# Kernel optimization log

Hardware: AMD Instinct MI355X
Metric: run time of the kernel (lower is better)

## Reference

```python
import jax, jax.numpy as jnp
import numpy as np

N_NODES = 50000
N_EDGES = 600000
DIM_H = 128
LN_EPS = 1e-5


def setup_inputs() -> dict:
    key = jax.random.key(0)
    ks = jax.random.split(key, 8)
    s = 1.0 / np.sqrt(DIM_H)
    return {
        "nodes": jax.random.normal(ks[0], (N_NODES, DIM_H), jnp.float32),
        "W_msg": jax.random.normal(ks[1], (DIM_H, DIM_H), jnp.float32) * s,
        "b_msg": jnp.zeros((DIM_H,), jnp.float32),
        "w_ih": jax.random.normal(ks[2], (3 * DIM_H, DIM_H), jnp.float32) * s,
        "w_hh": jax.random.normal(ks[3], (3 * DIM_H, DIM_H), jnp.float32) * s,
        "b_ih": jnp.zeros((3 * DIM_H,), jnp.float32),
        "b_hh": jnp.zeros((3 * DIM_H,), jnp.float32),
        "ln_gamma": jnp.ones((DIM_H,), jnp.float32),
        "ln_beta": jnp.zeros((DIM_H,), jnp.float32),
        "edge_src": jax.random.randint(ks[4], (N_EDGES,), 0, N_NODES, jnp.int32),
        "edge_dst": jax.random.randint(ks[5], (N_EDGES,), 0, N_NODES, jnp.int32),
    }


def _layer_norm(x, gamma, beta):
    mu = jnp.mean(x, axis=-1, keepdims=True)
    var = jnp.mean(jnp.square(x - mu), axis=-1, keepdims=True)
    return gamma * (x - mu) * jax.lax.rsqrt(var + LN_EPS) + beta


def reference(nodes, W_msg, b_msg, w_ih, w_hh, b_ih, b_hh, ln_gamma, ln_beta,
              edge_src, edge_dst):
    n_nodes = nodes.shape[0]
    # send_and_recv: per-edge message from source node, sum-reduce at dest
    msg_e = nodes[edge_src] @ W_msg.T + b_msg            # [E, H] (irregular gather)
    messages = jax.ops.segment_sum(msg_e, edge_dst, num_segments=n_nodes)  # [N, H]
    # global connection: add mean node feature
    msg = messages + jnp.mean(nodes, axis=0)
    # single-step GRU (torch gate layout: r, z, n)
    gi = msg @ w_ih.T + b_ih                             # [N, 3H]
    gh = nodes @ w_hh.T + b_hh                           # [N, 3H]
    i_r, i_z, i_n = jnp.split(gi, 3, axis=-1)
    h_r, h_z, h_n = jnp.split(gh, 3, axis=-1)
    r = jax.nn.sigmoid(i_r + h_r)
    z = jax.nn.sigmoid(i_z + h_z)
    n = jnp.tanh(i_n + r * h_n)
    h_next = (1.0 - z) * n + z * nodes
    # LayerNorm then post-GRU spatial residual with messages
    out = _layer_norm(h_next, ln_gamma, ln_beta)
    out = out + messages
    return out
```

## Files before the change

kernel.cpp:

```cpp
#include <hip/hip_runtime.h>
#include <hip/hip_bf16.h>

#define N_NODES 50000
#define N_EDGES 600000
#define DIM_H   128
#define NPAD    50048
#define NB_SCAN 196

typedef __attribute__((ext_vector_type(8))) short bf16x8;
typedef __attribute__((ext_vector_type(4))) float f32x4;
typedef __attribute__((ext_vector_type(4))) short short4v;

__device__ __forceinline__ short f2bs(float f) {
    __hip_bfloat16 h = __float2bfloat16(f);
    return *reinterpret_cast<short*>(&h);
}
__device__ __forceinline__ float bs2f(short s) {
    unsigned u = ((unsigned)(unsigned short)s) << 16;
    return __builtin_bit_cast(float, u);
}
__device__ __forceinline__ float sigm(float x) { return 1.f / (1.f + __expf(-x)); }
__device__ __forceinline__ float tanh_f(float x) {
    return 2.f / (1.f + __expf(-2.f * x)) - 1.f;
}
__device__ __forceinline__ unsigned pk2(float a, float b) {
    return ((unsigned)(unsigned short)f2bs(b) << 16) | (unsigned)(unsigned short)f2bs(a);
}
__device__ __forceinline__ float unlo(unsigned u) { return bs2f((short)(u & 0xffffu)); }
__device__ __forceinline__ float unhi(unsigned u) { return bs2f((short)(u >> 16)); }

__device__ __forceinline__ void dma16(const void* g, const void* lds_uniform) {
    __builtin_amdgcn_global_load_lds(
        (const __attribute__((address_space(1))) void*)g,
        (__attribute__((address_space(3))) void*)(unsigned)(unsigned long long)lds_uniform,
        16, 0, 0);
}

__global__ __launch_bounds__(256) void prep_k(const float* __restrict__ wmsg,
                                              const float* __restrict__ wih,
                                              const float* __restrict__ whh,
                                              short* __restrict__ wmsgB,
                                              short* __restrict__ wihB,
                                              short* __restrict__ whhB,
                                              int* __restrict__ cnt,
                                              float* __restrict__ colsum,
                                              short* __restrict__ aggTail,
                                              short* __restrict__ nodesTail) {
    int i = blockIdx.x * 256 + threadIdx.x;
    if (i < 16384) wmsgB[i] = f2bs(wmsg[i]);
    if (i < 49152) { wihB[i] = f2bs(wih[i]); whhB[i] = f2bs(whh[i]); }
    if (i < N_NODES) cnt[i] = 0;
    if (i < 128) colsum[i] = 0.f;
    if (i < 1536) {
        short4v z = {0, 0, 0, 0};
        *(short4v*)(aggTail   + i * 4) = z;
        *(short4v*)(nodesTail + i * 4) = z;
    }
}

__global__ __launch_bounds__(256) void colsum_k(const float* __restrict__ nodes,
                                                float* __restrict__ colsum,
                                                short* __restrict__ nodesB) {
    __shared__ float red[8][128];
    const int tid = threadIdx.x;
    const int cg = tid & 31;
    const int rl = tid >> 5;
    float4 acc = {0.f, 0.f, 0.f, 0.f};
    for (int r = blockIdx.x * 8 + rl; r < N_NODES; r += gridDim.x * 8) {
        float4 v = *(const float4*)(nodes + (size_t)r * DIM_H + cg * 4);
        acc.x += v.x; acc.y += v.y; acc.z += v.z; acc.w += v.w;
        *(short4v*)(nodesB + (size_t)r * DIM_H + cg * 4) =
            (short4v){f2bs(v.x), f2bs(v.y), f2bs(v.z), f2bs(v.w)};
    }
    *(float4*)&red[rl][cg * 4] = acc;
    __syncthreads();
    if (tid < 128) {
        float s = 0.f;
#pragma unroll
        for (int i = 0; i < 8; ++i) s += red[i][tid];
        unsafeAtomicAdd(&colsum[tid], s);
    }
}

__global__ __launch_bounds__(256) void hist_k(const int* __restrict__ edst,
                                              int* __restrict__ cnt) {
    int e = blockIdx.x * 256 + threadIdx.x;
    if (e < N_EDGES) atomicAdd(&cnt[edst[e]], 1);
}

__global__ __launch_bounds__(256) void bsum_k(const int* __restrict__ cnt,
                                              int* __restrict__ bsum) {
    const int t = threadIdx.x;
    int i = blockIdx.x * 256 + t;
    int v = (i < N_NODES) ? cnt[i] : 0;
#pragma unroll
    for (int o = 32; o; o >>= 1) v += __shfl_xor(v, o, 64);
    __shared__ int w4[4];
    if ((t & 63) == 0) w4[t >> 6] = v;
    __syncthreads();
    if (t == 0) bsum[blockIdx.x] = w4[0] + w4[1] + w4[2] + w4[3];
}

__global__ __launch_bounds__(256) void scan2_k(const int* __restrict__ cnt,
                                               const int* __restrict__ bsum,
                                               int* __restrict__ rowptr,
                                               int* __restrict__ pos) {
    const int b = blockIdx.x, t = threadIdx.x;
    const int lane = t & 63, w = t >> 6;
    __shared__ int red[4];
    __shared__ int wsum[4];

    int ov = (t < b) ? bsum[t] : 0;
#pragma unroll
    for (int o = 32; o; o >>= 1) ov += __shfl_xor(ov, o, 64);
    if (lane == 0) red[w] = ov;
    __syncthreads();
    const int offset = red[0] + red[1] + red[2] + red[3];

    int i = b * 256 + t;
    int v = (i < N_NODES) ? cnt[i] : 0;
    int x = v;
#pragma unroll
    for (int o = 1; o < 64; o <<= 1) {
        int y = __shfl_up(x, o, 64);
        if (lane >= o) x += y;
    }
    if (lane == 63) wsum[w] = x;
    __syncthreads();
    int woff = 0;
#pragma unroll
    for (int j = 0; j < 4; ++j)
        if (j < w) woff += wsum[j];
    int excl = offset + woff + (x - v);
    if (i < N_NODES) { rowptr[i] = excl; pos[i] = excl; }
    if (i == N_NODES - 1) rowptr[N_NODES] = excl + v;
}

__global__ __launch_bounds__(256) void reorder_k(const int* __restrict__ esrc,
                                                 const int* __restrict__ edst,
                                                 int* __restrict__ pos,
                                                 int* __restrict__ ssrc) {
    int e = blockIdx.x * 256 + threadIdx.x;
    if (e < N_EDGES) {
        int p = atomicAdd(&pos[edst[e]], 1);
        ssrc[p] = esrc[e];
    }
}

__global__ __launch_bounds__(256) void aggregate_k(const short* __restrict__ nodesB,
                                                   const int* __restrict__ rowptr,
                                                   const int* __restrict__ ssrc,
                                                   short* __restrict__ aggB) {
    const int wid = threadIdx.x >> 6;
    const int lane = threadIdx.x & 63;
    const int n = blockIdx.x * 4 + wid;
    if (n >= N_NODES) return;
    const int s0 = rowptr[n], s1 = rowptr[n + 1];
    float2 acc = {0.f, 0.f};
    int e = s0;
    for (; e + 3 < s1; e += 4) {
        int sa = ssrc[e], sb = ssrc[e + 1], sc = ssrc[e + 2], sd = ssrc[e + 3];
        short2 va = ((const short2*)(nodesB + (size_t)sa * DIM_H))[lane];
        short2 vb = ((const short2*)(nodesB + (size_t)sb * DIM_H))[lane];
        short2 vc = ((const short2*)(nodesB + (size_t)sc * DIM_H))[lane];
        short2 vd = ((const short2*)(nodesB + (size_t)sd * DIM_H))[lane];
        acc.x += (bs2f(va.x) + bs2f(vb.x)) + (bs2f(vc.x) + bs2f(vd.x));
        acc.y += (bs2f(va.y) + bs2f(vb.y)) + (bs2f(vc.y) + bs2f(vd.y));
    }
    for (; e < s1; ++e) {
        int sa = ssrc[e];
        short2 va = ((const short2*)(nodesB + (size_t)sa * DIM_H))[lane];
        acc.x += bs2f(va.x);
        acc.y += bs2f(va.y);
    }
    short2 o; o.x = f2bs(acc.x); o.y = f2bs(acc.y);
    ((short2*)(aggB + (size_t)n * DIM_H))[lane] = o;
}

__global__ __launch_bounds__(256) void fused_k(const short* __restrict__ aggB,
                                               const short* __restrict__ nodesB,
                                               const short* __restrict__ wmsgB,
                                               const short* __restrict__ wihB,
                                               const short* __restrict__ whhB,
                                               const float* __restrict__ bmsg,
                                               const float* __restrict__ bih,
                                               const float* __restrict__ bhh,
                                               const int* __restrict__ deg,
                                               const float* __restrict__ colsum,
                                               const float* __restrict__ gamma,
                                               const float* __restrict__ beta,
                                               float* __restrict__ out) {
    __shared__ short Ms[64 * 128];
    __shared__ short Wb[2][64 * 128];
    __shared__ float biasL[1280];

    const int tid = threadIdx.x;
    const int lane = tid & 63, w = tid >> 6;
    const int m0 = blockIdx.x * 64;
    const int r16 = lane & 15, qh = lane >> 4;
    const int wm = w * 16;
    const float invN = 1.0f / N_NODES;

    for (int i = tid; i < 384; i += 256) {
        biasL[i]       = bih[i];
        biasL[384 + i] = bhh[i];
    }
    if (tid < 128) {
        biasL[768  + tid] = bmsg[tid];
        biasL[896  + tid] = colsum[tid] * invN;
        biasL[1024 + tid] = gamma[tid];
        biasL[1152 + tid] = beta[tid];
    }
    __syncthreads();

    bf16x8 aggF[4], nodF[4], msgF[4];
    const size_t rowA = (size_t)(m0 + wm + r16) * 128;
#pragma unroll
    for (int kt = 0; kt < 4; ++kt) {
        aggF[kt] = *(const bf16x8*)(aggB   + rowA + ((kt << 2) + qh) * 8);
        nodF[kt] = *(const bf16x8*)(nodesB + rowA + ((kt << 2) + qh) * 8);
    }
    int4 dgi = *(const int4*)(deg + m0 + wm + qh * 4);

#define STAGE_W(SRC, ROW0, BUF) do {                                         \
    _Pragma("unroll") for (int it = 0; it < 4; ++it) {                       \
        int c = w * 4 + it;                                                  \
        int s = c * 64 + lane;                                               \
        int r = s >> 4, q = s & 15;                                          \
        int g = q ^ (r & 15);                                                \
        dma16((SRC) + (((size_t)((ROW0) + r)) << 7) + (g << 3),              \
              &Wb[BUF][0] + (size_t)c * 512);                                \
    } } while (0)

    STAGE_W(wmsgB, 0, 0);

    f32x4 acc[2][4];
    unsigned rp[2][4][2], inp[2][4][2], np_[2][4][2];

#define CHUNK(BUF, AF, H, RST) do {                                          \
    _Pragma("unroll") for (int kt = 0; kt < 4; ++kt) {                       \
        const int sq = (((kt << 2) + qh) ^ r16) << 3;                        \
        bf16x8 b0 = *(const bf16x8*)&Wb[BUF][(r16     ) * 128 + sq];         \
        bf16x8 b1 = *(const bf16x8*)&Wb[BUF][(r16 + 16) * 128 + sq];         \
        bf16x8 b2 = *(const bf16x8*)&Wb[BUF][(r16 + 32) * 128 + sq];         \
        bf16x8 b3 = *(const bf16x8*)&Wb[BUF][(r16 + 48) * 128 + sq];         \
        f32x4 z4 = {0.f, 0.f, 0.f, 0.f};                                     \
        acc[H][0] = __builtin_amdgcn_mfma_f32_16x16x32_bf16(                 \
            AF[kt], b0, ((RST) && kt == 0) ? z4 : acc[H][0], 0, 0, 0);       \
        acc[H][1] = __builtin_amdgcn_mfma_f32_16x16x32_bf16(                 \
            AF[kt], b1, ((RST) && kt == 0) ? z4 : acc[H][1], 0, 0, 0);       \
        acc[H][2] = __builtin_amdgcn_mfma_f32_16x16x32_bf16(                 \
            AF[kt], b2, ((RST) && kt == 0) ? z4 : acc[H][2], 0, 0, 0);       \
        acc[H][3] = __builtin_amdgcn_mfma_f32_16x16x32_bf16(                 \
            AF[kt], b3, ((RST) && kt == 0) ? z4 : acc[H][3], 0, 0, 0);       \
    } } while (0)

    __syncthreads(); STAGE_W(wmsgB,  64, 1); CHUNK(0, aggF, 0, 1);
    __syncthreads(); STAGE_W(wihB,    0, 0); CHUNK(1, aggF, 1, 1);

    {
        float dgf[4];
        dgf[0] = (m0 + wm + qh * 4 + 0 < N_NODES) ? (float)dgi.x : 0.f;
        dgf[1] = (m0 + wm + qh * 4 + 1 < N_NODES) ? (float)dgi.y : 0.f;
        dgf[2] = (m0 + wm + qh * 4 + 2 < N_NODES) ? (float)dgi.z : 0.f;
        dgf[3] = (m0 + wm + qh * 4 + 3 < N_NODES) ? (float)dgi.w : 0.f;
#pragma unroll
        for (int h = 0; h < 2; ++h)
#pragma unroll
            for (int j = 0; j < 4; ++j) {
                int c = h * 64 + j * 16 + r16;
                float bm = biasL[768 + c], cs = biasL[896 + c];
#pragma unroll
                for (int rr = 0; rr < 4; ++rr) {
                    int lr = wm + qh * 4 + rr;
                    float v = acc[h][j][rr] + dgf[rr] * bm + cs;
                    int slot = (c >> 3) ^ (lr & 15);
                    Ms[lr * 128 + slot * 8 + (c & 7)] = f2bs(v);
                }
            }
#pragma unroll
        for (int kt = 0; kt < 4; ++kt) {
            int kg = (kt << 2) + qh;
            msgF[kt] = *(const bf16x8*)&Ms[(wm + r16) * 128 + ((kg ^ r16) << 3)];
        }
    }

    __syncthreads(); STAGE_W(wihB,   64, 1); CHUNK(0, msgF, 0, 1);
    __syncthreads(); STAGE_W(whhB,    0, 0); CHUNK(1, msgF, 1, 1);
    __syncthreads(); STAGE_W(whhB,   64, 1); CHUNK(0, nodF, 0, 0);
    __syncthreads(); STAGE_W(wihB,  256, 0); CHUNK(1, nodF, 1, 0);
#pragma unroll
    for (int h = 0; h < 2; ++h)
#pragma unroll
        for (int j = 0; j < 4; ++j) {
            int c = h * 64 + j * 16 + r16;
            float b0 = biasL[c] + biasL[384 + c];
            rp[h][j][0] = pk2(sigm(acc[h][j][0] + b0), sigm(acc[h][j][1] + b0));
            rp[h][j][1] = pk2(sigm(acc[h][j][2] + b0), sigm(acc[h][j][3] + b0));
        }

    __syncthreads(); STAGE_W(wihB,  320, 1); CHUNK(0, msgF, 0, 1);
    __syncthreads(); STAGE_W(whhB,  256, 0); CHUNK(1, msgF, 1, 1);
#pragma unroll
    for (int h = 0; h < 2; ++h)
#pragma unroll
        for (int j = 0; j < 4; ++j) {
            int c = h * 64 + j * 16 + r16;
            float bi = biasL[256 + c];
            inp[h][j][0] = pk2(acc[h][j][0] + bi, acc[h][j][1] + bi);
            inp[h][j][1] = pk2(acc[h][j][2] + bi, acc[h][j][3] + bi);
        }

    __syncthreads(); STAGE_W(whhB,  320, 1); CHUNK(0, nodF, 0, 1);
    __syncthreads(); STAGE_W(wihB,  128, 0); CHUNK(1, nodF, 1, 1);
#pragma unroll
    for (int h = 0; h < 2; ++h)
#pragma unroll
        for (int j = 0; j < 4; ++j) {
            int c = h * 64 + j * 16 + r16;
            float bh = biasL[640 + c];
            float n0 = tanh_f(unlo(inp[h][j][0]) + unlo(rp[h][j][0]) * (acc[h][j][0] + bh));
            float n1 = tanh_f(unhi(inp[h][j][0]) + unhi(rp[h][j][0]) * (acc[h][j][1] + bh));
            float n2 = tanh_f(unlo(inp[h][j][1]) + unlo(rp[h][j][1]) * (acc[h][j][2] + bh));
            float n3 = tanh_f(unhi(inp[h][j][1]) + unhi(rp[h][j][1]) * (acc[h][j][3] + bh));
            np_[h][j][0] = pk2(n0, n1);
            np_[h][j][1] = pk2(n2, n3);
        }

    __syncthreads(); STAGE_W(wihB,  192, 1); CHUNK(0, msgF, 0, 1);
    __syncthreads(); STAGE_W(whhB,  128, 0); CHUNK(1, msgF, 1, 1);
    __syncthreads(); STAGE_W(whhB,  192, 1); CHUNK(0, nodF, 0, 0);
    __syncthreads();                         CHUNK(1, nodF, 1, 0);

#pragma unroll
    for (int h = 0; h < 2; ++h)
#pragma unroll
        for (int j = 0; j < 4; ++j) {
            int c = h * 64 + j * 16 + r16;
            float b1 = biasL[128 + c] + biasL[512 + c];
#pragma unroll
            for (int rr = 0; rr < 4; ++rr) {
                int lr = wm + qh * 4 + rr;
                float hv = bs2f(nodesB[(size_t)(m0 + lr) * 128 + c]);
                float z = sigm(acc[h][j][rr] + b1);
                float nv = (rr & 1) ? unhi(np_[h][j][rr >> 1]) : unlo(np_[h][j][rr >> 1]);
                acc[h][j][rr] = (1.f - z) * nv + z * hv;
            }
        }

#pragma unroll
    for (int rr = 0; rr < 4; ++rr) {
        float s = 0.f, q2 = 0.f;
#pragma unroll
        for (int h = 0; h < 2; ++h)
#pragma unroll
            for (int j = 0; j < 4; ++j) {
                float v = acc[h][j][rr];
                s += v; q2 += v * v;
            }
#pragma unroll
        for (int o = 1; o < 16; o <<= 1) {
            s  += __shfl_xor(s, o, 64);
            q2 += __shfl_xor(q2, o, 64);
        }
        int lr = wm + qh * 4 + rr;
        int gm = m0 + lr;
        float mu = s * (1.0f / DIM_H);
        float var = q2 * (1.0f / DIM_H) - mu * mu;
        float rstd = rsqrtf(var + 1e-5f);
        if (gm < N_NODES) {
#pragma unroll
            for (int h = 0; h < 2; ++h)
#pragma unroll
                for (int j = 0; j < 4; ++j) {
                    int c = h * 64 + j * 16 + r16;
                    int slot = (c >> 3) ^ (lr & 15);
                    float resid = bs2f(Ms[lr * 128 + slot * 8 + (c & 7)])
                                - biasL[896 + c];
                    out[(size_t)gm * DIM_H + c] =
                        biasL[1024 + c] * (acc[h][j][rr] - mu) * rstd
                        + biasL[1152 + c] + resid;
                }
        }
    }
#undef CHUNK
#undef STAGE_W
}

extern "C" void kernel_launch(void* const* d_in, const int* in_sizes, int n_in,
                              void* d_out, int out_size, void* d_ws, size_t ws_size,
                              hipStream_t stream) {
    const float* nodes = (const float*)d_in[0];
    const float* Wmsg  = (const float*)d_in[1];
    const float* bmsg  = (const float*)d_in[2];
    const float* wih   = (const float*)d_in[3];
    const float* whh   = (const float*)d_in[4];
    const float* bih   = (const float*)d_in[5];
    const float* bhh   = (const float*)d_in[6];
    const float* gamma = (const float*)d_in[7];
    const float* beta  = (const float*)d_in[8];
    const int* esrc = (const int*)d_in[9];
    const int* edst = (const int*)d_in[10];
    float* out = (float*)d_out;

    char* ws = (char*)d_ws;
    short* aggB   = (short*)ws;
    short* nodesB = (short*)(ws + 12812288);
    short* wmsgB  = (short*)(ws + 25624576);
    short* wihB   = (short*)(ws + 25657344);
    short* whhB   = (short*)(ws + 25755648);
    float* colsum = (float*)(ws + 25853952);
    int*   cnt    = (int*)(ws + 25854464);
    int*   rowptr = (int*)(ws + 26054464);
    int*   pos    = (int*)(ws + 26254480);
    int*   ssrc   = (int*)(ws + 26454480);
    int*   bsum   = (int*)(ws + 28854480);

    short* aggTail   = aggB   + (size_t)N_NODES * DIM_H;
    short* nodesTail = nodesB + (size_t)N_NODES * DIM_H;

    prep_k<<<NB_SCAN, 256, 0, stream>>>(Wmsg, wih, whh, wmsgB, wihB, whhB,
                                        cnt, colsum, aggTail, nodesTail);
    colsum_k<<<512, 256, 0, stream>>>(nodes, colsum, nodesB);

    const int EB = (N_EDGES + 255) / 256;
    hist_k<<<EB, 256, 0, stream>>>(edst, cnt);
    bsum_k<<<NB_SCAN, 256, 0, stream>>>(cnt, bsum);
    scan2_k<<<NB_SCAN, 256, 0, stream>>>(cnt, bsum, rowptr, pos);
    reorder_k<<<EB, 256, 0, stream>>>(esrc, edst, pos, ssrc);
    aggregate_k<<<(N_NODES + 3) / 4, 256, 0, stream>>>(nodesB, rowptr, ssrc, aggB);

    const int MB = (N_NODES + 63) / 64;
    fused_k<<<MB, 256, 0, stream>>>(aggB, nodesB, wmsgB, wihB, whhB,
                                    bmsg, bih, bhh, cnt, colsum, gamma, beta, out);
}
```

Before: 246.1 us.

## Triple-buffer weight staging with partial vmcnt waits and raw barriers

Expands the LDS weight buffer from two to three slots so each weight chunk is prefetched two steps ahead. Full __syncthreads are replaced with an s_waitcnt vmcnt(4) plus s_barrier, so only the older DMA group has to finish before the MFMA chunk runs. It also hoists the hidden-state gather for the GRU blend ahead of the final chunk so its latency overlaps with compute. The extra LDS per block may lower occupancy, and the hand-written vmcnt counts must match the number of outstanding loads exactly or the code reads stale weights.

```diff
diff --git a/kernel.cpp b/kernel.cpp
--- a/kernel.cpp
+++ b/kernel.cpp
@@ -191,7 +191,7 @@
                                                const float* __restrict__ beta,
                                                float* __restrict__ out) {
     __shared__ short Ms[64 * 128];
-    __shared__ short Wb[2][64 * 128];
+    __shared__ short Wb[3][64 * 128];
     __shared__ float biasL[1280];
 
     const int tid = threadIdx.x;
@@ -211,7 +211,6 @@
         biasL[1024 + tid] = gamma[tid];
         biasL[1152 + tid] = beta[tid];
     }
-    __syncthreads();
 
     bf16x8 aggF[4], nodF[4], msgF[4];
     const size_t rowA = (size_t)(m0 + wm + r16) * 128;
@@ -232,7 +231,16 @@
               &Wb[BUF][0] + (size_t)c * 512);                                \
     } } while (0)
 
-    STAGE_W(wmsgB, 0, 0);
+    STAGE_W(wmsgB,  0, 0);
+    STAGE_W(wmsgB, 64, 1);
+    __syncthreads();
+
+#define PBAR(NLIT) do {                                                      \
+    asm volatile("s_waitcnt vmcnt(" #NLIT ")" ::: "memory");                 \
+    __builtin_amdgcn_sched_barrier(0);                                       \
+    __builtin_amdgcn_s_barrier();                                            \
+    __builtin_amdgcn_sched_barrier(0);                                       \
+    } while (0)
 
     f32x4 acc[2][4];
     unsigned rp[2][4][2], inp[2][4][2], np_[2][4][2];
@@ -255,9 +263,8 @@
             AF[kt], b3, ((RST) && kt == 0) ? z4 : acc[H][3], 0, 0, 0);       \
     } } while (0)
 
-    __syncthreads(); STAGE_W(wmsgB,  64, 1); CHUNK(0, aggF, 0, 1);
-    __syncthreads(); STAGE_W(wihB,    0, 0); CHUNK(1, aggF, 1, 1);
-
+    STAGE_W(wihB,   0, 2);  CHUNK(0, aggF, 0, 1);
+    PBAR(4); STAGE_W(wihB,  64, 0);  CHUNK(1, aggF, 1, 1);
     {
         float dgf[4];
         dgf[0] = (m0 + wm + qh * 4 + 0 < N_NODES) ? (float)dgi.x : 0.f;
@@ -284,11 +291,10 @@
             msgF[kt] = *(const bf16x8*)&Ms[(wm + r16) * 128 + ((kg ^ r16) << 3)];
         }
     }
-
-    __syncthreads(); STAGE_W(wihB,   64, 1); CHUNK(0, msgF, 0, 1);
-    __syncthreads(); STAGE_W(whhB,    0, 0); CHUNK(1, msgF, 1, 1);
-    __syncthreads(); STAGE_W(whhB,   64, 1); CHUNK(0, nodF, 0, 0);
-    __syncthreads(); STAGE_W(wihB,  256, 0); CHUNK(1, nodF, 1, 0);
+    PBAR(4); STAGE_W(whhB,   0, 1);  CHUNK(2, msgF, 0, 1);
+    PBAR(4); STAGE_W(whhB,  64, 2);  CHUNK(0, msgF, 1, 1);
+    PBAR(4); STAGE_W(wihB, 256, 0);  CHUNK(1, nodF, 0, 0);
+    PBAR(4); STAGE_W(wihB, 320, 1);  CHUNK(2, nodF, 1, 0);
 #pragma unroll
     for (int h = 0; h < 2; ++h)
 #pragma unroll
@@ -298,9 +304,8 @@
             rp[h][j][0] = pk2(sigm(acc[h][j][0] + b0), sigm(acc[h][j][1] + b0));
             rp[h][j][1] = pk2(sigm(acc[h][j][2] + b0), sigm(acc[h][j][3] + b0));
         }
-
-    __syncthreads(); STAGE_W(wihB,  320, 1); CHUNK(0, msgF, 0, 1);
-    __syncthreads(); STAGE_W(whhB,  256, 0); CHUNK(1, msgF, 1, 1);
+    PBAR(4); STAGE_W(whhB, 256, 2);  CHUNK(0, msgF, 0, 1);
+    PBAR(4); STAGE_W(whhB, 320, 0);  CHUNK(1, msgF, 1, 1);
 #pragma unroll
     for (int h = 0; h < 2; ++h)
 #pragma unroll
@@ -310,9 +315,8 @@
             inp[h][j][0] = pk2(acc[h][j][0] + bi, acc[h][j][1] + bi);
             inp[h][j][1] = pk2(acc[h][j][2] + bi, acc[h][j][3] + bi);
         }
-
-    __syncthreads(); STAGE_W(whhB,  320, 1); CHUNK(0, nodF, 0, 1);
-    __syncthreads(); STAGE_W(wihB,  128, 0); CHUNK(1, nodF, 1, 1);
+    PBAR(4); STAGE_W(wihB, 128, 1);  CHUNK(2, nodF, 0, 1);
+    PBAR(4); STAGE_W(wihB, 192, 2);  CHUNK(0, nodF, 1, 1);
 #pragma unroll
     for (int h = 0; h < 2; ++h)
 #pragma unroll
@@ -326,12 +330,21 @@
             np_[h][j][0] = pk2(n0, n1);
             np_[h][j][1] = pk2(n2, n3);
         }
-
-    __syncthreads(); STAGE_W(wihB,  192, 1); CHUNK(0, msgF, 0, 1);
-    __syncthreads(); STAGE_W(whhB,  128, 0); CHUNK(1, msgF, 1, 1);
-    __syncthreads(); STAGE_W(whhB,  192, 1); CHUNK(0, nodF, 0, 0);
-    __syncthreads();                         CHUNK(1, nodF, 1, 0);
-
+    PBAR(4); STAGE_W(whhB, 128, 0);  CHUNK(1, msgF, 0, 1);
+    PBAR(4); STAGE_W(whhB, 192, 1);  CHUNK(2, msgF, 1, 1);
+    PBAR(4);                         CHUNK(0, nodF, 0, 0);
+    short hs[2][4][4];
+#pragma unroll
+    for (int h = 0; h < 2; ++h)
+#pragma unroll
+        for (int j = 0; j < 4; ++j)
+#pragma unroll
+            for (int rr = 0; rr < 4; ++rr) {
+                int lr = wm + qh * 4 + rr;
+                int c = h * 64 + j * 16 + r16;
+                hs[h][j][rr] = nodesB[(size_t)(m0 + lr) * 128 + c];
+            }
+    PBAR(32);                        CHUNK(1, nodF, 1, 0);
 #pragma unroll
     for (int h = 0; h < 2; ++h)
 #pragma unroll
@@ -340,8 +353,7 @@
             float b1 = biasL[128 + c] + biasL[512 + c];
 #pragma unroll
             for (int rr = 0; rr < 4; ++rr) {
-                int lr = wm + qh * 4 + rr;
-                float hv = bs2f(nodesB[(size_t)(m0 + lr) * 128 + c]);
+                float hv = bs2f(hs[h][j][rr]);
                 float z = sigm(acc[h][j][rr] + b1);
                 float nv = (rr & 1) ? unhi(np_[h][j][rr >> 1]) : unlo(np_[h][j][rr >> 1]);
                 acc[h][j][rr] = (1.f - z) * nv + z * hv;
@@ -384,6 +396,7 @@
         }
     }
 #undef CHUNK
+#undef PBAR
 #undef STAGE_W
 }
 
```

Result: slower. 261.5 us (+6.2%).

## Vectorize edge kernels and widen aggregation loads to 16-byte rows

Applied to the files above, without the earlier changes.

The histogram and reorder kernels now have each thread handle four edges through int4 loads, cutting the launch to a quarter of the blocks. The aggregation kernel splits each wave into four groups of sixteen lanes, each lane loading 8 bf16 values with one 16-byte load. The groups take interleaved edges and are then combined with cross-lane shuffles, which gives more independent gathers in flight. A __syncthreads after bias staging in the fused kernel is also removed; if later code reads biasL before another barrier, that is a race.

```diff
diff --git a/kernel.cpp b/kernel.cpp
--- a/kernel.cpp
+++ b/kernel.cpp
@@ -84,8 +84,14 @@
 
 __global__ __launch_bounds__(256) void hist_k(const int* __restrict__ edst,
                                               int* __restrict__ cnt) {
-    int e = blockIdx.x * 256 + threadIdx.x;
-    if (e < N_EDGES) atomicAdd(&cnt[edst[e]], 1);
+    int e = (blockIdx.x * 256 + threadIdx.x) * 4;
+    if (e + 3 < N_EDGES) {
+        int4 d = *(const int4*)(edst + e);
+        atomicAdd(&cnt[d.x], 1); atomicAdd(&cnt[d.y], 1);
+        atomicAdd(&cnt[d.z], 1); atomicAdd(&cnt[d.w], 1);
+    } else {
+        for (; e < N_EDGES; ++e) atomicAdd(&cnt[edst[e]], 1);
+    }
 }
 
 __global__ __launch_bounds__(256) void bsum_k(const int* __restrict__ cnt,
@@ -140,10 +146,19 @@
                                                  const int* __restrict__ edst,
                                                  int* __restrict__ pos,
                                                  int* __restrict__ ssrc) {
-    int e = blockIdx.x * 256 + threadIdx.x;
-    if (e < N_EDGES) {
-        int p = atomicAdd(&pos[edst[e]], 1);
-        ssrc[p] = esrc[e];
+    int e = (blockIdx.x * 256 + threadIdx.x) * 4;
+    if (e + 3 < N_EDGES) {
+        int4 s = *(const int4*)(esrc + e);
+        int4 d = *(const int4*)(edst + e);
+        ssrc[atomicAdd(&pos[d.x], 1)] = s.x;
+        ssrc[atomicAdd(&pos[d.y], 1)] = s.y;
+        ssrc[atomicAdd(&pos[d.z], 1)] = s.z;
+        ssrc[atomicAdd(&pos[d.w], 1)] = s.w;
+    } else {
+        for (; e < N_EDGES; ++e) {
+            int p = atomicAdd(&pos[edst[e]], 1);
+            ssrc[p] = esrc[e];
+        }
     }
 }
 
@@ -153,28 +168,39 @@
                                                    short* __restrict__ aggB) {
     const int wid = threadIdx.x >> 6;
     const int lane = threadIdx.x & 63;
+    const int g = lane >> 4, l = lane & 15;
     const int n = blockIdx.x * 4 + wid;
     if (n >= N_NODES) return;
     const int s0 = rowptr[n], s1 = rowptr[n + 1];
-    float2 acc = {0.f, 0.f};
-    int e = s0;
-    for (; e + 3 < s1; e += 4) {
-        int sa = ssrc[e], sb = ssrc[e + 1], sc = ssrc[e + 2], sd = ssrc[e + 3];
-        short2 va = ((const short2*)(nodesB + (size_t)sa * DIM_H))[lane];
-        short2 vb = ((const short2*)(nodesB + (size_t)sb * DIM_H))[lane];
-        short2 vc = ((const short2*)(nodesB + (size_t)sc * DIM_H))[lane];
-        short2 vd = ((const short2*)(nodesB + (size_t)sd * DIM_H))[lane];
-        acc.x += (bs2f(va.x) + bs2f(vb.x)) + (bs2f(vc.x) + bs2f(vd.x));
-        acc.y += (bs2f(va.y) + bs2f(vb.y)) + (bs2f(vc.y) + bs2f(vd.y));
-    }
-    for (; e < s1; ++e) {
+
+    float accf[8] = {0.f, 0.f, 0.f, 0.f, 0.f, 0.f, 0.f, 0.f};
+    int e = s0 + g;
+    for (; e + 4 < s1; e += 8) {
+        int sa = ssrc[e], sb = ssrc[e + 4];
+        bf16x8 va = *(const bf16x8*)(nodesB + (size_t)sa * DIM_H + l * 8);
+        bf16x8 vb = *(const bf16x8*)(nodesB + (size_t)sb * DIM_H + l * 8);
+#pragma unroll
+        for (int k = 0; k < 8; ++k) accf[k] += bs2f(va[k]) + bs2f(vb[k]);
+    }
+    if (e < s1) {
         int sa = ssrc[e];
-        short2 va = ((const short2*)(nodesB + (size_t)sa * DIM_H))[lane];
-        acc.x += bs2f(va.x);
-        acc.y += bs2f(va.y);
-    }
-    short2 o; o.x = f2bs(acc.x); o.y = f2bs(acc.y);
-    ((short2*)(aggB + (size_t)n * DIM_H))[lane] = o;
+        bf16x8 va = *(const bf16x8*)(nodesB + (size_t)sa * DIM_H + l * 8);
+#pragma unroll
+        for (int k = 0; k < 8; ++k) accf[k] += bs2f(va[k]);
+    }
+#pragma unroll
+    for (int k = 0; k < 8; ++k) {
+        accf[k] += __shfl_xor(accf[k], 32, 64);
+        accf[k] += __shfl_xor(accf[k], 16, 64);
+    }
+    if (g == 0) {
+        uint4 ov;
+        ov.x = pk2(accf[0], accf[1]);
+        ov.y = pk2(accf[2], accf[3]);
+        ov.z = pk2(accf[4], accf[5]);
+        ov.w = pk2(accf[6], accf[7]);
+        *(uint4*)(aggB + (size_t)n * DIM_H + l * 8) = ov;
+    }
 }
 
 __global__ __launch_bounds__(256) void fused_k(const short* __restrict__ aggB,
@@ -211,7 +237,6 @@
         biasL[1024 + tid] = gamma[tid];
         biasL[1152 + tid] = beta[tid];
     }
-    __syncthreads();
 
     bf16x8 aggF[4], nodF[4], msgF[4];
     const size_t rowA = (size_t)(m0 + wm + r16) * 128;
@@ -423,11 +448,11 @@
                                         cnt, colsum, aggTail, nodesTail);
     colsum_k<<<512, 256, 0, stream>>>(nodes, colsum, nodesB);
 
-    const int EB = (N_EDGES + 255) / 256;
-    hist_k<<<EB, 256, 0, stream>>>(edst, cnt);
+    const int EB4 = (N_EDGES / 4 + 255) / 256;
+    hist_k<<<EB4, 256, 0, stream>>>(edst, cnt);
     bsum_k<<<NB_SCAN, 256, 0, stream>>>(cnt, bsum);
     scan2_k<<<NB_SCAN, 256, 0, stream>>>(cnt, bsum, rowptr, pos);
-    reorder_k<<<EB, 256, 0, stream>>>(esrc, edst, pos, ssrc);
+    reorder_k<<<EB4, 256, 0, stream>>>(esrc, edst, pos, ssrc);
     aggregate_k<<<(N_NODES + 3) / 4, 256, 0, stream>>>(nodesB, rowptr, ssrc, aggB);
 
     const int MB = (N_NODES + 63) / 64;
```

New measurement: 236.2 us. 4.0% less time.
